# Performance work log

Measured on AMD Instinct MI355X. Metric: run time of the kernel, lower is better.

## Reference

```python
import jax, jax.numpy as jnp
import numpy as np

N_NODES = 50000
N_EDGES = 1600000
IN_DIM = 512
HID = 128  # conv1 out = 2*HID = 256, conv2 out = HID = 128
EPS = 1e-5


def gcn_conv(x, src, dst, W, b, n_nodes):
    """PyG GCNConv: x' = D^{-1/2} (A + I) D^{-1/2} (x W) + b (self loops added)."""
    h = x @ W  # [N, out]
    loop = jnp.arange(n_nodes, dtype=src.dtype)
    s = jnp.concatenate([src, loop])  # sources incl. self loops
    d = jnp.concatenate([dst, loop])  # targets incl. self loops
    ones = jnp.ones(s.shape[0], dtype=h.dtype)
    deg = jax.ops.segment_sum(ones, d, num_segments=n_nodes)  # in-degree on targets
    dis = jnp.where(deg > 0, jax.lax.rsqrt(jnp.maximum(deg, 1.0)), 0.0)
    norm = dis[s] * dis[d]  # [E+N]
    msg = norm[:, None] * h[s]  # gather + scale, [E+N, out]
    out = jax.ops.segment_sum(msg, d, num_segments=n_nodes)  # scatter-add
    return out + b


def batch_norm(x, gamma, beta):
    """BatchNorm1d with batch statistics (biased variance), eps=1e-5."""
    mean = jnp.mean(x, axis=0)
    var = jnp.mean(jnp.square(x - mean), axis=0)
    return (x - mean) * jax.lax.rsqrt(var + EPS) * gamma + beta


def setup_inputs() -> dict:
    key = jax.random.key(0)
    ks = jax.random.split(key, 8)
    x = jax.random.normal(ks[0], (N_NODES, IN_DIM), dtype=jnp.float32)
    edge_index = jax.random.randint(ks[1], (2, N_EDGES), 0, N_NODES, dtype=jnp.int64)
    d1 = 2 * HID
    W1 = jax.random.normal(ks[2], (IN_DIM, d1), dtype=jnp.float32) / np.sqrt(IN_DIM)
    b1 = jnp.zeros((d1,), dtype=jnp.float32)
    gamma1 = jnp.ones((d1,), dtype=jnp.float32)
    beta1 = jnp.zeros((d1,), dtype=jnp.float32)
    W2 = jax.random.normal(ks[3], (d1, HID), dtype=jnp.float32) / np.sqrt(d1)
    b2 = jnp.zeros((HID,), dtype=jnp.float32)
    gamma2 = jnp.ones((HID,), dtype=jnp.float32)
    beta2 = jnp.zeros((HID,), dtype=jnp.float32)
    return {"x": x, "edge_index": edge_index, "W1": W1, "b1": b1,
            "gamma1": gamma1, "beta1": beta1, "W2": W2, "b2": b2,
            "gamma2": gamma2, "beta2": beta2}


def reference(x, edge_index, W1, b1, gamma1, beta1, W2, b2, gamma2, beta2):
    src, dst = edge_index[0], edge_index[1]
    h = gcn_conv(x, src, dst, W1, b1, N_NODES)
    h = batch_norm(h, gamma1, beta1)
    h = jax.nn.relu(h)
    # dropout: identity in eval mode (deterministic reference)
    h = gcn_conv(h, src, dst, W2, b2, N_NODES)
    h = batch_norm(h, gamma2, beta2)
    return h
```

## Files before the change

kernel.cpp:

```cpp
#include <hip/hip_runtime.h>
#include <hip/hip_bf16.h>


#define NN 50000
#define NE 1600000
#define DIN 512
#define D1 256
#define D2 128
#define EPSV 1e-5f
#define NBUCK 8
#define BSZ 6250
#define NDB 128
#define NPB 391
#define CAP 16384

typedef __attribute__((ext_vector_type(8))) short bf16x8_t;
typedef __attribute__((ext_vector_type(4))) float f32x4_t;

__device__ __forceinline__ float bf2f(unsigned short u) {
  return __uint_as_float(((unsigned int)u) << 16);
}
__device__ __forceinline__ unsigned short f2bf(float f) {
  unsigned int u = __float_as_uint(f);
  u += 0x7fffu + ((u >> 16) & 1u);
  return (unsigned short)(u >> 16);
}
__device__ __forceinline__ unsigned int pk2(float a, float b) {
  __hip_bfloat162 h = __float22bfloat162_rn(make_float2(a, b));
  union { __hip_bfloat162 h; unsigned int u; } c;
  c.h = h;
  return c.u;
}

__global__ void k_zero(int* __restrict__ gcursor, float* __restrict__ stats) {
  int i = blockIdx.x * 256 + threadIdx.x;
  if (i < NDB) gcursor[i] = 0;
  if (i < (D1 * 2 + D2 * 2)) stats[i] = 0.0f;
}

__global__ __launch_bounds__(256) void k_part(const int* __restrict__ src,
                                              const int* __restrict__ dst,
                                              int* __restrict__ gcursor,
                                              unsigned int* __restrict__ part) {
  __shared__ int hist[NDB];
  __shared__ int curs[NDB];
  const int t = threadIdx.x;
  const int EB = NE / 256;
  const int e0 = blockIdx.x * EB;
  if (t < NDB) hist[t] = 0;
  __syncthreads();
  for (int i = t; i < EB; i += 256) {
    int d = dst[e0 + i];
    atomicAdd(&hist[d / NPB], 1);
  }
  __syncthreads();
  if (t < NDB) {
    int c = hist[t];
    curs[t] = (c > 0) ? atomicAdd(&gcursor[t], c) : 0;
  }
  __syncthreads();
  for (int i = t; i < EB; i += 256) {
    int s = src[e0 + i];
    int d = dst[e0 + i];
    int b = d / NPB;
    int dl = d - b * NPB;
    int sb = (unsigned)s / BSZ;
    unsigned int w = (unsigned)s | ((unsigned)dl << 16) | ((unsigned)sb << 25);
    int pos = atomicAdd(&curs[b], 1);
    if (pos < CAP) part[(size_t)b * CAP + pos] = w;
  }
}

__global__ void k_bscan(const int* __restrict__ gcursor, int* __restrict__ ebase) {
  __shared__ int s[NDB];
  int t = threadIdx.x;
  int v = gcursor[t];
  s[t] = v;
  __syncthreads();
  for (int off = 1; off < NDB; off <<= 1) {
    int a = (t >= off) ? s[t - off] : 0;
    __syncthreads();
    s[t] += a;
    __syncthreads();
  }
  ebase[t] = s[t] - v;
  if (t == NDB - 1) ebase[NDB] = s[t];
}

__global__ __launch_bounds__(256) void k_build(const unsigned int* __restrict__ part,
                                               const int* __restrict__ gcursor,
                                               const int* __restrict__ ebase,
                                               int* __restrict__ row_ptr,
                                               float* __restrict__ dis,
                                               int* __restrict__ col) {
  const int NC = NPB * NBUCK;
  __shared__ int cnt[NC];
  __shared__ int tsum[256];
  const int b = blockIdx.x, t = threadIdx.x;
  int m = gcursor[b];
  if (m > CAP) m = CAP;
  const int base = ebase[b];
  const unsigned int* my = part + (size_t)b * CAP;
  for (int i = t; i < NC; i += 256) cnt[i] = 0;
  __syncthreads();
  for (int i = t; i < m; i += 256) {
    unsigned int w = my[i];
    atomicAdd(&cnt[((w >> 16) & 0x1ff) * NBUCK + (w >> 25)], 1);
  }
  __syncthreads();
  const int CHK = (NC + 255) / 256;
  int i0 = t * CHK;
  int sum = 0;
  for (int i = 0; i < CHK; i++) {
    int idx = i0 + i;
    if (idx < NC) sum += cnt[idx];
  }
  tsum[t] = sum;
  __syncthreads();
  for (int off = 1; off < 256; off <<= 1) {
    int a = (t >= off) ? tsum[t - off] : 0;
    __syncthreads();
    tsum[t] += a;
    __syncthreads();
  }
  int run = tsum[t] - sum;
  for (int i = 0; i < CHK; i++) {
    int idx = i0 + i;
    if (idx < NC) {
      int c = cnt[idx];
      cnt[idx] = run;
      run += c;
    }
  }
  __syncthreads();
  const int n0 = b * NPB;
  for (int dl = t; dl < NPB; dl += 256) {
    int n = n0 + dl;
    if (n < NN) {
      int st = cnt[dl * NBUCK];
      int en = (dl * NBUCK + NBUCK < NC) ? cnt[dl * NBUCK + NBUCK] : m;
      row_ptr[n] = base + st;
      dis[n] = rsqrtf((float)(en - st + 1));
    }
  }
  if (b == NDB - 1 && t == 0) row_ptr[NN] = base + m;
  __syncthreads();
  for (int i = t; i < m; i += 256) {
    unsigned int w = my[i];
    int pos = atomicAdd(&cnt[((w >> 16) & 0x1ff) * NBUCK + (w >> 25)], 1);
    col[base + pos] = w & 0xffff;
  }
}

__global__ void k_prep_w(const float* __restrict__ W1, const float* __restrict__ W2,
                         unsigned short* __restrict__ W1t, unsigned short* __restrict__ W2t) {
  int i = blockIdx.x * 256 + threadIdx.x;
  if (i < DIN * D1) {
    int n = i / DIN, k = i - n * DIN;
    W1t[i] = f2bf(W1[(size_t)k * D1 + n]);
  } else {
    int j = i - DIN * D1;
    int n = j / D1, k = j - n * D1;
    W2t[j] = f2bf(W2[(size_t)k * D2 + n]);
  }
}

__global__ __launch_bounds__(512) void k_gemm1(const float* __restrict__ A,
                                               const unsigned short* __restrict__ Bt,
                                               unsigned short* __restrict__ C, int M) {
  __shared__ unsigned short As[128 * 64];
  __shared__ unsigned short Bs[256 * 64];
  const int t = threadIdx.x;
  const int wave = t >> 6, lane = t & 63;
  const int m0 = blockIdx.x * 128;
  const int wm = (wave & 1) * 64, wn = (wave >> 1) * 64;
  const int l8 = lane >> 3;
  const int lbs = (lane & 7) ^ l8;
  const int row_c = lane & 15, quad = lane >> 4;

  f32x4_t acc[4][4];
#pragma unroll
  for (int i = 0; i < 4; i++)
#pragma unroll
    for (int j = 0; j < 4; j++) acc[i][j] = (f32x4_t){0.f, 0.f, 0.f, 0.f};

  for (int k0 = 0; k0 < DIN; k0 += 64) {
#pragma unroll
    for (int j = 0; j < 4; j++) {
      int chunk = wave * 4 + j;
      int row = chunk * 8 + l8;
      const unsigned short* g = Bt + (size_t)row * DIN + k0 + lbs * 8;
      __builtin_amdgcn_global_load_lds(
          (const __attribute__((address_space(1))) unsigned int*)g,
          (__attribute__((address_space(3))) unsigned int*)(Bs + chunk * 512), 16, 0, 0);
    }
#pragma unroll
    for (int i = 0; i < 2; i++) {
      int bid = i * 512 + t;
      int row = bid >> 3, pb = bid & 7;
      int lb = pb ^ (row & 7);
      int gm = m0 + row;
      if (gm >= M) gm = M - 1;
      const float4* s = (const float4*)(A + (size_t)gm * DIN + k0 + lb * 8);
      float4 v0 = s[0], v1 = s[1];
      uint4 o;
      o.x = pk2(v0.x, v0.y);
      o.y = pk2(v0.z, v0.w);
      o.z = pk2(v1.x, v1.y);
      o.w = pk2(v1.z, v1.w);
      *(uint4*)(As + row * 64 + pb * 8) = o;
    }
    __syncthreads();
#pragma unroll
    for (int ki = 0; ki < 2; ki++) {
      bf16x8_t af[4], bfr[4];
      int kb = ki * 4 + quad;
#pragma unroll
      for (int i = 0; i < 4; i++) {
        int ar = wm + i * 16 + row_c;
        af[i] = *(const bf16x8_t*)(As + ar * 64 + ((kb ^ (ar & 7)) * 8));
        int br = wn + i * 16 + row_c;
        bfr[i] = *(const bf16x8_t*)(Bs + br * 64 + ((kb ^ (br & 7)) * 8));
      }
#pragma unroll
      for (int i = 0; i < 4; i++)
#pragma unroll
        for (int j = 0; j < 4; j++)
          acc[i][j] = __builtin_amdgcn_mfma_f32_16x16x32_bf16(af[i], bfr[j], acc[i][j], 0, 0, 0);
    }
    __syncthreads();
  }
#pragma unroll
  for (int i = 0; i < 4; i++) {
#pragma unroll
    for (int j = 0; j < 4; j++) {
      int colv = wn + j * 16 + row_c;
#pragma unroll
      for (int r = 0; r < 4; r++) {
        int gm = m0 + wm + i * 16 + quad * 4 + r;
        if (gm < M) C[(size_t)gm * D1 + colv] = f2bf(acc[i][j][r]);
      }
    }
  }
}

__global__ void k_finalize1(const float* __restrict__ stats, const float* __restrict__ gamma,
                            const float* __restrict__ beta, float* __restrict__ sc1,
                            float* __restrict__ sh1) {
  int c = threadIdx.x;
  float mean = stats[c] * (1.0f / NN);
  float var = stats[D1 + c] * (1.0f / NN) - mean * mean;
  float sc = gamma[c] * rsqrtf(var + EPSV);
  sc1[c] = sc;
  sh1[c] = beta[c] - mean * sc;
}

__global__ __launch_bounds__(256) void k_gemm2(const unsigned short* __restrict__ A,
                                               const float* __restrict__ sc1,
                                               const float* __restrict__ sh1,
                                               const unsigned short* __restrict__ Bt,
                                               unsigned short* __restrict__ C, int M) {
  __shared__ unsigned short As[128 * 64];
  __shared__ unsigned short Bs[128 * 64];
  const int t = threadIdx.x;
  const int wave = t >> 6, lane = t & 63;
  const int m0 = blockIdx.x * 128;
  const int wm = (wave >> 1) * 64, wn = (wave & 1) * 64;
  const int l8 = lane >> 3;
  const int lbs = (lane & 7) ^ l8;
  const int row_c = lane & 15, quad = lane >> 4;

  f32x4_t acc[4][4];
#pragma unroll
  for (int i = 0; i < 4; i++)
#pragma unroll
    for (int j = 0; j < 4; j++) acc[i][j] = (f32x4_t){0.f, 0.f, 0.f, 0.f};

  for (int k0 = 0; k0 < D1; k0 += 64) {
#pragma unroll
    for (int j = 0; j < 4; j++) {
      int chunk = wave * 4 + j;
      int row = chunk * 8 + l8;
      const unsigned short* g = Bt + (size_t)row * D1 + k0 + lbs * 8;
      __builtin_amdgcn_global_load_lds(
          (const __attribute__((address_space(1))) unsigned int*)g,
          (__attribute__((address_space(3))) unsigned int*)(Bs + chunk * 512), 16, 0, 0);
    }
#pragma unroll
    for (int i = 0; i < 4; i++) {
      int bid = i * 256 + t;
      int row = bid >> 3, pb = bid & 7;
      int lb = pb ^ (row & 7);
      int gm = m0 + row;
      if (gm >= M) gm = M - 1;
      int colb = k0 + lb * 8;
      uint4 raw = *(const uint4*)(A + (size_t)gm * D1 + colb);
      float4 scA = *(const float4*)(sc1 + colb);
      float4 scB = *(const float4*)(sc1 + colb + 4);
      float4 shA = *(const float4*)(sh1 + colb);
      float4 shB = *(const float4*)(sh1 + colb + 4);
      float f0 = fmaxf(fmaf(bf2f((unsigned short)(raw.x & 0xffff)), scA.x, shA.x), 0.f);
      float f1 = fmaxf(fmaf(bf2f((unsigned short)(raw.x >> 16)),    scA.y, shA.y), 0.f);
      float f2 = fmaxf(fmaf(bf2f((unsigned short)(raw.y & 0xffff)), scA.z, shA.z), 0.f);
      float f3 = fmaxf(fmaf(bf2f((unsigned short)(raw.y >> 16)),    scA.w, shA.w), 0.f);
      float f4 = fmaxf(fmaf(bf2f((unsigned short)(raw.z & 0xffff)), scB.x, shB.x), 0.f);
      float f5 = fmaxf(fmaf(bf2f((unsigned short)(raw.z >> 16)),    scB.y, shB.y), 0.f);
      float f6 = fmaxf(fmaf(bf2f((unsigned short)(raw.w & 0xffff)), scB.z, shB.z), 0.f);
      float f7 = fmaxf(fmaf(bf2f((unsigned short)(raw.w >> 16)),    scB.w, shB.w), 0.f);
      uint4 o;
      o.x = pk2(f0, f1);
      o.y = pk2(f2, f3);
      o.z = pk2(f4, f5);
      o.w = pk2(f6, f7);
      *(uint4*)(As + row * 64 + pb * 8) = o;
    }
    __syncthreads();
#pragma unroll
    for (int ki = 0; ki < 2; ki++) {
      bf16x8_t af[4], bfr[4];
      int kb = ki * 4 + quad;
#pragma unroll
      for (int i = 0; i < 4; i++) {
        int ar = wm + i * 16 + row_c;
        af[i] = *(const bf16x8_t*)(As + ar * 64 + ((kb ^ (ar & 7)) * 8));
        int br = wn + i * 16 + row_c;
        bfr[i] = *(const bf16x8_t*)(Bs + br * 64 + ((kb ^ (br & 7)) * 8));
      }
#pragma unroll
      for (int i = 0; i < 4; i++)
#pragma unroll
        for (int j = 0; j < 4; j++)
          acc[i][j] = __builtin_amdgcn_mfma_f32_16x16x32_bf16(af[i], bfr[j], acc[i][j], 0, 0, 0);
    }
    __syncthreads();
  }
#pragma unroll
  for (int i = 0; i < 4; i++) {
#pragma unroll
    for (int j = 0; j < 4; j++) {
      int colv = wn + j * 16 + row_c;
      if (colv < D2) {
#pragma unroll
        for (int r = 0; r < 4; r++) {
          int gm = m0 + wm + i * 16 + quad * 4 + r;
          if (gm < M) C[(size_t)gm * D2 + colv] = f2bf(acc[i][j][r]);
        }
      }
    }
  }
}

__global__ __launch_bounds__(256) void k_agg1(const unsigned short* __restrict__ H,
                                              const int* __restrict__ row_ptr,
                                              const int* __restrict__ col,
                                              const float* __restrict__ dis,
                                              const float* __restrict__ bias,
                                              unsigned short* __restrict__ OUT) {
  int n = blockIdx.x * 4 + (threadIdx.x >> 6);
  int lane = threadIdx.x & 63;
  if (n >= NN) return;
  float dn = dis[n];
  ushort4 v = ((const ushort4*)(H + (size_t)n * D1))[lane];
  float wsf = dn * dn;
  float a0 = wsf * bf2f(v.x), a1 = wsf * bf2f(v.y);
  float a2 = wsf * bf2f(v.z), a3 = wsf * bf2f(v.w);
  int e = row_ptr[n], e1 = row_ptr[n + 1];
  for (; e + 3 < e1; e += 4) {
    int s0 = col[e], s1 = col[e + 1], s2 = col[e + 2], s3 = col[e + 3];
    float w0 = dis[s0] * dn, w1 = dis[s1] * dn;
    float w2 = dis[s2] * dn, w3 = dis[s3] * dn;
    ushort4 u0 = ((const ushort4*)(H + (size_t)s0 * D1))[lane];
    ushort4 u1 = ((const ushort4*)(H + (size_t)s1 * D1))[lane];
    ushort4 u2 = ((const ushort4*)(H + (size_t)s2 * D1))[lane];
    ushort4 u3 = ((const ushort4*)(H + (size_t)s3 * D1))[lane];
    a0 += w0 * bf2f(u0.x) + w1 * bf2f(u1.x) + w2 * bf2f(u2.x) + w3 * bf2f(u3.x);
    a1 += w0 * bf2f(u0.y) + w1 * bf2f(u1.y) + w2 * bf2f(u2.y) + w3 * bf2f(u3.y);
    a2 += w0 * bf2f(u0.z) + w1 * bf2f(u1.z) + w2 * bf2f(u2.z) + w3 * bf2f(u3.z);
    a3 += w0 * bf2f(u0.w) + w1 * bf2f(u1.w) + w2 * bf2f(u2.w) + w3 * bf2f(u3.w);
  }
  for (; e < e1; e++) {
    int sa = col[e];
    float wa = dis[sa] * dn;
    ushort4 ua = ((const ushort4*)(H + (size_t)sa * D1))[lane];
    a0 += wa * bf2f(ua.x);
    a1 += wa * bf2f(ua.y);
    a2 += wa * bf2f(ua.z);
    a3 += wa * bf2f(ua.w);
  }
  int c = lane * 4;
  a0 += bias[c]; a1 += bias[c + 1]; a2 += bias[c + 2]; a3 += bias[c + 3];
  ushort4 o;
  o.x = f2bf(a0); o.y = f2bf(a1); o.z = f2bf(a2); o.w = f2bf(a3);
  ((ushort4*)(OUT + (size_t)n * D1))[lane] = o;
}

__global__ __launch_bounds__(256) void k_agg2(const unsigned short* __restrict__ H,
                                              const int* __restrict__ row_ptr,
                                              const int* __restrict__ col,
                                              const float* __restrict__ dis,
                                              const float* __restrict__ bias,
                                              float* __restrict__ OUT) {
  int n = blockIdx.x * 4 + (threadIdx.x >> 6);
  int lane = threadIdx.x & 63;
  if (n >= NN) return;
  float dn = dis[n];
  ushort2 v = ((const ushort2*)(H + (size_t)n * D2))[lane];
  float wsf = dn * dn;
  float a0 = wsf * bf2f(v.x), a1 = wsf * bf2f(v.y);
  int e = row_ptr[n], e1 = row_ptr[n + 1];
  for (; e + 3 < e1; e += 4) {
    int s0 = col[e], s1 = col[e + 1], s2 = col[e + 2], s3 = col[e + 3];
    float w0 = dis[s0] * dn, w1 = dis[s1] * dn;
    float w2 = dis[s2] * dn, w3 = dis[s3] * dn;
    ushort2 u0 = ((const ushort2*)(H + (size_t)s0 * D2))[lane];
    ushort2 u1 = ((const ushort2*)(H + (size_t)s1 * D2))[lane];
    ushort2 u2 = ((const ushort2*)(H + (size_t)s2 * D2))[lane];
    ushort2 u3 = ((const ushort2*)(H + (size_t)s3 * D2))[lane];
    a0 += w0 * bf2f(u0.x) + w1 * bf2f(u1.x) + w2 * bf2f(u2.x) + w3 * bf2f(u3.x);
    a1 += w0 * bf2f(u0.y) + w1 * bf2f(u1.y) + w2 * bf2f(u2.y) + w3 * bf2f(u3.y);
  }
  for (; e < e1; e++) {
    int sa = col[e];
    float wa = dis[sa] * dn;
    ushort2 ua = ((const ushort2*)(H + (size_t)sa * D2))[lane];
    a0 += wa * bf2f(ua.x);
    a1 += wa * bf2f(ua.y);
  }
  int c = lane * 2;
  a0 += bias[c]; a1 += bias[c + 1];
  ((float2*)(OUT + (size_t)n * D2))[lane] = make_float2(a0, a1);
}

__global__ void k_stats1(const unsigned short* __restrict__ X, float* __restrict__ stats) {
  int t = threadIdx.x;
  int r0 = blockIdx.x * 64;
  int r1 = (r0 + 64 < NN) ? r0 + 64 : NN;
  float s = 0.f, q = 0.f;
  for (int r = r0; r < r1; r++) {
    float v = bf2f(X[(size_t)r * D1 + t]);
    s += v;
    q += v * v;
  }
  atomicAdd(&stats[t], s);
  atomicAdd(&stats[D1 + t], q);
}

__global__ void k_stats2(const float* __restrict__ X, float* __restrict__ stats) {
  int t = threadIdx.x;
  int r0 = blockIdx.x * 128;
  int r1 = (r0 + 128 < NN) ? r0 + 128 : NN;
  float s = 0.f, q = 0.f;
  for (int r = r0; r < r1; r++) {
    float v = X[(size_t)r * D2 + t];
    s += v;
    q += v * v;
  }
  atomicAdd(&stats[t], s);
  atomicAdd(&stats[D2 + t], q);
}

__global__ void k_apply2(float* __restrict__ X, const float* __restrict__ stats,
                         const float* __restrict__ gamma, const float* __restrict__ beta) {
  int i = blockIdx.x * blockDim.x + threadIdx.x;
  int c = i & (D2 - 1);
  float mean = stats[c] * (1.0f / NN);
  float var = stats[D2 + c] * (1.0f / NN) - mean * mean;
  float sc = gamma[c] * rsqrtf(var + EPSV);
  X[i] = (X[i] - mean) * sc + beta[c];
}

extern "C" void kernel_launch(void* const* d_in, const int* in_sizes, int n_in,
                              void* d_out, int out_size, void* d_ws, size_t ws_size,
                              hipStream_t stream) {
  const float* x  = (const float*)d_in[0];
  const int* ei   = (const int*)d_in[1];
  const int* srcv = ei;
  const int* dstv = ei + NE;
  const float* W1  = (const float*)d_in[2];
  const float* b1  = (const float*)d_in[3];
  const float* g1  = (const float*)d_in[4];
  const float* be1 = (const float*)d_in[5];
  const float* W2  = (const float*)d_in[6];
  const float* b2  = (const float*)d_in[7];
  const float* g2  = (const float*)d_in[8];
  const float* be2 = (const float*)d_in[9];
  float* out = (float*)d_out;

  char* ws = (char*)d_ws;
  size_t off = 0;
  auto alloc = [&](size_t bytes) {
    size_t cur = off;
    off = (off + bytes + 255) & ~(size_t)255;
    return cur;
  };
  int* row_ptr   = (int*)(ws + alloc((NN + 1) * 4));
  float* dis     = (float*)(ws + alloc(NN * 4));
  int* gcursor   = (int*)(ws + alloc(NDB * 4));
  int* ebase     = (int*)(ws + alloc((NDB + 1) * 4));
  float* stats   = (float*)(ws + alloc((D1 * 2 + D2 * 2) * 4));
  float* sc1     = (float*)(ws + alloc(D1 * 4));
  float* sh1     = (float*)(ws + alloc(D1 * 4));
  int* col       = (int*)(ws + alloc((size_t)NE * 4));
  unsigned short* H1  = (unsigned short*)(ws + alloc((size_t)NN * D1 * 2));
  unsigned short* A1  = (unsigned short*)(ws + alloc((size_t)NN * D1 * 2));
  unsigned short* H2  = (unsigned short*)(ws + alloc((size_t)NN * D2 * 2));
  unsigned short* W1t = (unsigned short*)(ws + alloc((size_t)DIN * D1 * 2));
  unsigned short* W2t = (unsigned short*)(ws + alloc((size_t)D1 * D2 * 2));
  float* stats2 = stats + D1 * 2;
  unsigned int* part = (unsigned int*)H1;

  k_zero<<<3, 256, 0, stream>>>(gcursor, stats);
  k_part<<<256, 256, 0, stream>>>(srcv, dstv, gcursor, part);
  k_bscan<<<1, NDB, 0, stream>>>(gcursor, ebase);
  k_build<<<NDB, 256, 0, stream>>>(part, gcursor, ebase, row_ptr, dis, col);

  k_prep_w<<<(DIN * D1 + D1 * D2) / 256, 256, 0, stream>>>(W1, W2, W1t, W2t);

  const int mb = (NN + 127) / 128;

  k_gemm1<<<mb, 512, 0, stream>>>(x, W1t, H1, NN);
  k_agg1<<<(NN + 3) / 4, 256, 0, stream>>>(H1, row_ptr, col, dis, b1, A1);
  k_stats1<<<(NN + 63) / 64, 256, 0, stream>>>(A1, stats);
  k_finalize1<<<1, 256, 0, stream>>>(stats, g1, be1, sc1, sh1);

  k_gemm2<<<mb, 256, 0, stream>>>(A1, sc1, sh1, W2t, H2, NN);
  k_agg2<<<(NN + 3) / 4, 256, 0, stream>>>(H2, row_ptr, col, dis, b2, out);
  k_stats2<<<(NN + 127) / 128, 128, 0, stream>>>(out, stats2);
  k_apply2<<<NN * D2 / 256, 256, 0, stream>>>(out, stats2, g2, be2);
}
```

Measured before the change: 529.8 us.

## Cooperatively load edge indices per wave and broadcast via readlane in aggregation

In both aggregation kernels, each wave now loads up to 64 neighbor indices and their normalization weights in one coalesced load, one per lane. It then broadcasts them with readlane and issues 8 row gathers at a time. This replaces the redundant per-lane loads of col and dis and raises memory-level parallelism for the gathers. It also doubles the bucket count and halves the bucket size used by the CSR build, which changes the sort/partition granularity. The cost is more registers per thread and some extra readlane instructions.

```diff
diff --git a/kernel.cpp b/kernel.cpp
--- a/kernel.cpp
+++ b/kernel.cpp
@@ -8,8 +8,8 @@
 #define D1 256
 #define D2 128
 #define EPSV 1e-5f
-#define NBUCK 8
-#define BSZ 6250
+#define NBUCK 16
+#define BSZ 3125
 #define NDB 128
 #define NPB 391
 #define CAP 16384
@@ -365,27 +365,44 @@
   float a0 = wsf * bf2f(v.x), a1 = wsf * bf2f(v.y);
   float a2 = wsf * bf2f(v.z), a3 = wsf * bf2f(v.w);
   int e = row_ptr[n], e1 = row_ptr[n + 1];
-  for (; e + 3 < e1; e += 4) {
-    int s0 = col[e], s1 = col[e + 1], s2 = col[e + 2], s3 = col[e + 3];
-    float w0 = dis[s0] * dn, w1 = dis[s1] * dn;
-    float w2 = dis[s2] * dn, w3 = dis[s3] * dn;
-    ushort4 u0 = ((const ushort4*)(H + (size_t)s0 * D1))[lane];
-    ushort4 u1 = ((const ushort4*)(H + (size_t)s1 * D1))[lane];
-    ushort4 u2 = ((const ushort4*)(H + (size_t)s2 * D1))[lane];
-    ushort4 u3 = ((const ushort4*)(H + (size_t)s3 * D1))[lane];
-    a0 += w0 * bf2f(u0.x) + w1 * bf2f(u1.x) + w2 * bf2f(u2.x) + w3 * bf2f(u3.x);
-    a1 += w0 * bf2f(u0.y) + w1 * bf2f(u1.y) + w2 * bf2f(u2.y) + w3 * bf2f(u3.y);
-    a2 += w0 * bf2f(u0.z) + w1 * bf2f(u1.z) + w2 * bf2f(u2.z) + w3 * bf2f(u3.z);
-    a3 += w0 * bf2f(u0.w) + w1 * bf2f(u1.w) + w2 * bf2f(u2.w) + w3 * bf2f(u3.w);
-  }
-  for (; e < e1; e++) {
-    int sa = col[e];
-    float wa = dis[sa] * dn;
-    ushort4 ua = ((const ushort4*)(H + (size_t)sa * D1))[lane];
-    a0 += wa * bf2f(ua.x);
-    a1 += wa * bf2f(ua.y);
-    a2 += wa * bf2f(ua.z);
-    a3 += wa * bf2f(ua.w);
+  while (e < e1) {
+    int cnt = e1 - e;
+    if (cnt > 64) cnt = 64;
+    int li = (lane < cnt) ? lane : (cnt - 1);
+    int cv = col[e + li];
+    float dwv = dis[cv] * dn;
+    int dwu = __float_as_int(dwv);
+    int b = 0;
+    for (; b + 8 <= cnt; b += 8) {
+      int s[8];
+      float w[8];
+      ushort4 u[8];
+#pragma unroll
+      for (int k = 0; k < 8; k++) {
+        s[k] = __builtin_amdgcn_readlane(cv, b + k);
+        w[k] = __int_as_float(__builtin_amdgcn_readlane(dwu, b + k));
+      }
+#pragma unroll
+      for (int k = 0; k < 8; k++)
+        u[k] = ((const ushort4*)(H + (size_t)s[k] * D1))[lane];
+#pragma unroll
+      for (int k = 0; k < 8; k++) {
+        a0 += w[k] * bf2f(u[k].x);
+        a1 += w[k] * bf2f(u[k].y);
+        a2 += w[k] * bf2f(u[k].z);
+        a3 += w[k] * bf2f(u[k].w);
+      }
+    }
+    for (; b < cnt; b++) {
+      int sK = __builtin_amdgcn_readlane(cv, b);
+      float wK = __int_as_float(__builtin_amdgcn_readlane(dwu, b));
+      ushort4 uK = ((const ushort4*)(H + (size_t)sK * D1))[lane];
+      a0 += wK * bf2f(uK.x);
+      a1 += wK * bf2f(uK.y);
+      a2 += wK * bf2f(uK.z);
+      a3 += wK * bf2f(uK.w);
+    }
+    e += cnt;
   }
   int c = lane * 4;
   a0 += bias[c]; a1 += bias[c + 1]; a2 += bias[c + 2]; a3 += bias[c + 3];
@@ -408,23 +425,40 @@
   float wsf = dn * dn;
   float a0 = wsf * bf2f(v.x), a1 = wsf * bf2f(v.y);
   int e = row_ptr[n], e1 = row_ptr[n + 1];
-  for (; e + 3 < e1; e += 4) {
-    int s0 = col[e], s1 = col[e + 1], s2 = col[e + 2], s3 = col[e + 3];
-    float w0 = dis[s0] * dn, w1 = dis[s1] * dn;
-    float w2 = dis[s2] * dn, w3 = dis[s3] * dn;
-    ushort2 u0 = ((const ushort2*)(H + (size_t)s0 * D2))[lane];
-    ushort2 u1 = ((const ushort2*)(H + (size_t)s1 * D2))[lane];
-    ushort2 u2 = ((const ushort2*)(H + (size_t)s2 * D2))[lane];
-    ushort2 u3 = ((const ushort2*)(H + (size_t)s3 * D2))[lane];
-    a0 += w0 * bf2f(u0.x) + w1 * bf2f(u1.x) + w2 * bf2f(u2.x) + w3 * bf2f(u3.x);
-    a1 += w0 * bf2f(u0.y) + w1 * bf2f(u1.y) + w2 * bf2f(u2.y) + w3 * bf2f(u3.y);
-  }
-  for (; e < e1; e++) {
-    int sa = col[e];
-    float wa = dis[sa] * dn;
-    ushort2 ua = ((const ushort2*)(H + (size_t)sa * D2))[lane];
-    a0 += wa * bf2f(ua.x);
-    a1 += wa * bf2f(ua.y);
+  while (e < e1) {
+    int cnt = e1 - e;
+    if (cnt > 64) cnt = 64;
+    int li = (lane < cnt) ? lane : (cnt - 1);
+    int cv = col[e + li];
+    float dwv = dis[cv] * dn;
+    int dwu = __float_as_int(dwv);
+    int b = 0;
+    for (; b + 8 <= cnt; b += 8) {
+      int s[8];
+      float w[8];
+      ushort2 u[8];
+#pragma unroll
+      for (int k = 0; k < 8; k++) {
+        s[k] = __builtin_amdgcn_readlane(cv, b + k);
+        w[k] = __int_as_float(__builtin_amdgcn_readlane(dwu, b + k));
+      }
+#pragma unroll
+      for (int k = 0; k < 8; k++)
+        u[k] = ((const ushort2*)(H + (size_t)s[k] * D2))[lane];
+#pragma unroll
+      for (int k = 0; k < 8; k++) {
+        a0 += w[k] * bf2f(u[k].x);
+        a1 += w[k] * bf2f(u[k].y);
+      }
+    }
+    for (; b < cnt; b++) {
+      int sK = __builtin_amdgcn_readlane(cv, b);
+      float wK = __int_as_float(__builtin_amdgcn_readlane(dwu, b));
+      ushort2 uK = ((const ushort2*)(H + (size_t)sK * D2))[lane];
+      a0 += wK * bf2f(uK.x);
+      a1 += wK * bf2f(uK.y);
+    }
+    e += cnt;
   }
   int c = lane * 2;
   a0 += bias[c]; a1 += bias[c + 1];
```

Result: faster. 512.9 us (-3.2%).

## Aggregate many nodes per wave bucket-by-bucket for source locality

Applied to the files above, without the earlier changes.

The CSR build now records per-node boundaries for 16 source buckets instead of a single row pointer. Each aggregation wave owns 13 destination nodes and walks all of them one source bucket at a time, with block-wide barriers between buckets. The aim is to keep concurrently gathered source rows in a narrow range so they hit L2/MALL, and to fold the destination normalisation into the epilogue. The cost is a larger boundary array, heavy register use for 13 accumulators per wave, a much smaller grid that gives less parallelism, and barrier stalls that can leave waves waiting.

```diff
diff --git a/kernel.cpp b/kernel.cpp
--- a/kernel.cpp
+++ b/kernel.cpp
@@ -8,11 +8,14 @@
 #define D1 256
 #define D2 128
 #define EPSV 1e-5f
-#define NBUCK 8
-#define BSZ 6250
+#define NBUCK 16
+#define BSZ 3125
 #define NDB 128
 #define NPB 391
 #define CAP 16384
+
+#define AGG_KN 13
+#define AGG_GRID ((NN + AGG_KN * 4 - 1) / (AGG_KN * 4))
 
 typedef __attribute__((ext_vector_type(8))) short bf16x8_t;
 typedef __attribute__((ext_vector_type(4))) float f32x4_t;
@@ -90,7 +93,7 @@
 __global__ __launch_bounds__(256) void k_build(const unsigned int* __restrict__ part,
                                                const int* __restrict__ gcursor,
                                                const int* __restrict__ ebase,
-                                               int* __restrict__ row_ptr,
+                                               int* __restrict__ bptr,
                                                float* __restrict__ dis,
                                                int* __restrict__ col) {
   const int NC = NPB * NBUCK;
@@ -134,16 +137,20 @@
   }
   __syncthreads();
   const int n0 = b * NPB;
+  for (int i = t; i < NC; i += 256) {
+    int dl = i >> 4;
+    int n = n0 + dl;
+    if (n < NN) bptr[(size_t)n * NBUCK + (i & 15)] = base + cnt[i];
+  }
   for (int dl = t; dl < NPB; dl += 256) {
     int n = n0 + dl;
     if (n < NN) {
       int st = cnt[dl * NBUCK];
       int en = (dl * NBUCK + NBUCK < NC) ? cnt[dl * NBUCK + NBUCK] : m;
-      row_ptr[n] = base + st;
       dis[n] = rsqrtf((float)(en - st + 1));
     }
   }
-  if (b == NDB - 1 && t == 0) row_ptr[NN] = base + m;
+  if (b == NDB - 1 && t == 0) bptr[(size_t)NN * NBUCK] = base + m;
   __syncthreads();
   for (int i = t; i < m; i += 256) {
     unsigned int w = my[i];
@@ -350,85 +357,165 @@
   }
 }
 
-__global__ __launch_bounds__(256) void k_agg1(const unsigned short* __restrict__ H,
-                                              const int* __restrict__ row_ptr,
-                                              const int* __restrict__ col,
-                                              const float* __restrict__ dis,
-                                              const float* __restrict__ bias,
-                                              unsigned short* __restrict__ OUT) {
-  int n = blockIdx.x * 4 + (threadIdx.x >> 6);
-  int lane = threadIdx.x & 63;
-  if (n >= NN) return;
-  float dn = dis[n];
-  ushort4 v = ((const ushort4*)(H + (size_t)n * D1))[lane];
-  float wsf = dn * dn;
-  float a0 = wsf * bf2f(v.x), a1 = wsf * bf2f(v.y);
-  float a2 = wsf * bf2f(v.z), a3 = wsf * bf2f(v.w);
-  int e = row_ptr[n], e1 = row_ptr[n + 1];
-  for (; e + 3 < e1; e += 4) {
-    int s0 = col[e], s1 = col[e + 1], s2 = col[e + 2], s3 = col[e + 3];
-    float w0 = dis[s0] * dn, w1 = dis[s1] * dn;
-    float w2 = dis[s2] * dn, w3 = dis[s3] * dn;
-    ushort4 u0 = ((const ushort4*)(H + (size_t)s0 * D1))[lane];
-    ushort4 u1 = ((const ushort4*)(H + (size_t)s1 * D1))[lane];
-    ushort4 u2 = ((const ushort4*)(H + (size_t)s2 * D1))[lane];
-    ushort4 u3 = ((const ushort4*)(H + (size_t)s3 * D1))[lane];
-    a0 += w0 * bf2f(u0.x) + w1 * bf2f(u1.x) + w2 * bf2f(u2.x) + w3 * bf2f(u3.x);
-    a1 += w0 * bf2f(u0.y) + w1 * bf2f(u1.y) + w2 * bf2f(u2.y) + w3 * bf2f(u3.y);
-    a2 += w0 * bf2f(u0.z) + w1 * bf2f(u1.z) + w2 * bf2f(u2.z) + w3 * bf2f(u3.z);
-    a3 += w0 * bf2f(u0.w) + w1 * bf2f(u1.w) + w2 * bf2f(u2.w) + w3 * bf2f(u3.w);
-  }
-  for (; e < e1; e++) {
-    int sa = col[e];
-    float wa = dis[sa] * dn;
-    ushort4 ua = ((const ushort4*)(H + (size_t)sa * D1))[lane];
-    a0 += wa * bf2f(ua.x);
-    a1 += wa * bf2f(ua.y);
-    a2 += wa * bf2f(ua.z);
-    a3 += wa * bf2f(ua.w);
-  }
-  int c = lane * 4;
-  a0 += bias[c]; a1 += bias[c + 1]; a2 += bias[c + 2]; a3 += bias[c + 3];
-  ushort4 o;
-  o.x = f2bf(a0); o.y = f2bf(a1); o.z = f2bf(a2); o.w = f2bf(a3);
-  ((ushort4*)(OUT + (size_t)n * D1))[lane] = o;
-}
-
-__global__ __launch_bounds__(256) void k_agg2(const unsigned short* __restrict__ H,
-                                              const int* __restrict__ row_ptr,
-                                              const int* __restrict__ col,
-                                              const float* __restrict__ dis,
-                                              const float* __restrict__ bias,
-                                              float* __restrict__ OUT) {
-  int n = blockIdx.x * 4 + (threadIdx.x >> 6);
-  int lane = threadIdx.x & 63;
-  if (n >= NN) return;
-  float dn = dis[n];
-  ushort2 v = ((const ushort2*)(H + (size_t)n * D2))[lane];
-  float wsf = dn * dn;
-  float a0 = wsf * bf2f(v.x), a1 = wsf * bf2f(v.y);
-  int e = row_ptr[n], e1 = row_ptr[n + 1];
-  for (; e + 3 < e1; e += 4) {
-    int s0 = col[e], s1 = col[e + 1], s2 = col[e + 2], s3 = col[e + 3];
-    float w0 = dis[s0] * dn, w1 = dis[s1] * dn;
-    float w2 = dis[s2] * dn, w3 = dis[s3] * dn;
-    ushort2 u0 = ((const ushort2*)(H + (size_t)s0 * D2))[lane];
-    ushort2 u1 = ((const ushort2*)(H + (size_t)s1 * D2))[lane];
-    ushort2 u2 = ((const ushort2*)(H + (size_t)s2 * D2))[lane];
-    ushort2 u3 = ((const ushort2*)(H + (size_t)s3 * D2))[lane];
-    a0 += w0 * bf2f(u0.x) + w1 * bf2f(u1.x) + w2 * bf2f(u2.x) + w3 * bf2f(u3.x);
-    a1 += w0 * bf2f(u0.y) + w1 * bf2f(u1.y) + w2 * bf2f(u2.y) + w3 * bf2f(u3.y);
-  }
-  for (; e < e1; e++) {
-    int sa = col[e];
-    float wa = dis[sa] * dn;
-    ushort2 ua = ((const ushort2*)(H + (size_t)sa * D2))[lane];
-    a0 += wa * bf2f(ua.x);
-    a1 += wa * bf2f(ua.y);
-  }
-  int c = lane * 2;
-  a0 += bias[c]; a1 += bias[c + 1];
-  ((float2*)(OUT + (size_t)n * D2))[lane] = make_float2(a0, a1);
+__global__ __launch_bounds__(256, 4) void k_agg1(const unsigned short* __restrict__ H,
+                                                 const int* __restrict__ bptr,
+                                                 const int* __restrict__ col,
+                                                 const float* __restrict__ dis,
+                                                 const float* __restrict__ bias,
+                                                 unsigned short* __restrict__ OUT) {
+  const int lane = threadIdx.x & 63;
+  const int wid = blockIdx.x * 4 + (threadIdx.x >> 6);
+  const int n0 = wid * AGG_KN;
+
+  float a0[AGG_KN], a1[AGG_KN], a2[AGG_KN], a3[AGG_KN];
+  int bnd[AGG_KN];
+
+#pragma unroll
+  for (int j = 0; j < AGG_KN; j++) {
+    int n = n0 + j;
+    if (n < NN) {
+      float d = dis[n];
+      ushort4 v = ((const ushort4*)(H + (size_t)n * D1))[lane];
+      a0[j] = d * bf2f(v.x); a1[j] = d * bf2f(v.y);
+      a2[j] = d * bf2f(v.z); a3[j] = d * bf2f(v.w);
+      int li = (lane <= NBUCK) ? lane : NBUCK;
+      bnd[j] = bptr[(size_t)n * NBUCK + li];
+    } else {
+      a0[j] = a1[j] = a2[j] = a3[j] = 0.f;
+      bnd[j] = 0;
+    }
+  }
+
+  for (int b = 0; b < NBUCK; b++) {
+#pragma unroll
+    for (int j = 0; j < AGG_KN; j++) {
+      int s = __builtin_amdgcn_readlane(bnd[j], b);
+      int e = __builtin_amdgcn_readlane(bnd[j], b + 1);
+      for (; s + 4 <= e; s += 4) {
+        int c0 = col[s], c1 = col[s + 1], c2 = col[s + 2], c3 = col[s + 3];
+        float w0 = dis[c0], w1 = dis[c1], w2 = dis[c2], w3 = dis[c3];
+        ushort4 u0 = ((const ushort4*)(H + (size_t)c0 * D1))[lane];
+        ushort4 u1 = ((const ushort4*)(H + (size_t)c1 * D1))[lane];
+        ushort4 u2 = ((const ushort4*)(H + (size_t)c2 * D1))[lane];
+        ushort4 u3 = ((const ushort4*)(H + (size_t)c3 * D1))[lane];
+        a0[j] += w0 * bf2f(u0.x) + w1 * bf2f(u1.x) + w2 * bf2f(u2.x) + w3 * bf2f(u3.x);
+        a1[j] += w0 * bf2f(u0.y) + w1 * bf2f(u1.y) + w2 * bf2f(u2.y) + w3 * bf2f(u3.y);
+        a2[j] += w0 * bf2f(u0.z) + w1 * bf2f(u1.z) + w2 * bf2f(u2.z) + w3 * bf2f(u3.z);
+        a3[j] += w0 * bf2f(u0.w) + w1 * bf2f(u1.w) + w2 * bf2f(u2.w) + w3 * bf2f(u3.w);
+      }
+      if (s + 2 <= e) {
+        int c0 = col[s], c1 = col[s + 1];
+        float w0 = dis[c0], w1 = dis[c1];
+        ushort4 u0 = ((const ushort4*)(H + (size_t)c0 * D1))[lane];
+        ushort4 u1 = ((const ushort4*)(H + (size_t)c1 * D1))[lane];
+        a0[j] += w0 * bf2f(u0.x) + w1 * bf2f(u1.x);
+        a1[j] += w0 * bf2f(u0.y) + w1 * bf2f(u1.y);
+        a2[j] += w0 * bf2f(u0.z) + w1 * bf2f(u1.z);
+        a3[j] += w0 * bf2f(u0.w) + w1 * bf2f(u1.w);
+        s += 2;
+      }
+      if (s < e) {
+        int c0 = col[s];
+        float w0 = dis[c0];
+        ushort4 u0 = ((const ushort4*)(H + (size_t)c0 * D1))[lane];
+        a0[j] += w0 * bf2f(u0.x);
+        a1[j] += w0 * bf2f(u0.y);
+        a2[j] += w0 * bf2f(u0.z);
+        a3[j] += w0 * bf2f(u0.w);
+      }
+    }
+    __syncthreads();
+  }
+
+  float4 bb = ((const float4*)bias)[lane];
+#pragma unroll
+  for (int j = 0; j < AGG_KN; j++) {
+    int n = n0 + j;
+    if (n < NN) {
+      float d = dis[n];
+      ushort4 o;
+      o.x = f2bf(fmaf(d, a0[j], bb.x));
+      o.y = f2bf(fmaf(d, a1[j], bb.y));
+      o.z = f2bf(fmaf(d, a2[j], bb.z));
+      o.w = f2bf(fmaf(d, a3[j], bb.w));
+      ((ushort4*)(OUT + (size_t)n * D1))[lane] = o;
+    }
+  }
+}
+
+__global__ __launch_bounds__(256, 4) void k_agg2(const unsigned short* __restrict__ H,
+                                                 const int* __restrict__ bptr,
+                                                 const int* __restrict__ col,
+                                                 const float* __restrict__ dis,
+                                                 const float* __restrict__ bias,
+                                                 float* __restrict__ OUT) {
+  const int lane = threadIdx.x & 63;
+  const int wid = blockIdx.x * 4 + (threadIdx.x >> 6);
+  const int n0 = wid * AGG_KN;
+
+  float a0[AGG_KN], a1[AGG_KN];
+  int bnd[AGG_KN];
+
+#pragma unroll
+  for (int j = 0; j < AGG_KN; j++) {
+    int n = n0 + j;
+    if (n < NN) {
+      float d = dis[n];
+      ushort2 v = ((const ushort2*)(H + (size_t)n * D2))[lane];
+      a0[j] = d * bf2f(v.x); a1[j] = d * bf2f(v.y);
+      int li = (lane <= NBUCK) ? lane : NBUCK;
+      bnd[j] = bptr[(size_t)n * NBUCK + li];
+    } else {
+      a0[j] = a1[j] = 0.f;
+      bnd[j] = 0;
+    }
+  }
+
+  for (int b = 0; b < NBUCK; b++) {
+#pragma unroll
+    for (int j = 0; j < AGG_KN; j++) {
+      int s = __builtin_amdgcn_readlane(bnd[j], b);
+      int e = __builtin_amdgcn_readlane(bnd[j], b + 1);
+      for (; s + 4 <= e; s += 4) {
+        int c0 = col[s], c1 = col[s + 1], c2 = col[s + 2], c3 = col[s + 3];
+        float w0 = dis[c0], w1 = dis[c1], w2 = dis[c2], w3 = dis[c3];
+        ushort2 u0 = ((const ushort2*)(H + (size_t)c0 * D2))[lane];
+        ushort2 u1 = ((const ushort2*)(H + (size_t)c1 * D2))[lane];
+        ushort2 u2 = ((const ushort2*)(H + (size_t)c2 * D2))[lane];
+        ushort2 u3 = ((const ushort2*)(H + (size_t)c3 * D2))[lane];
+        a0[j] += w0 * bf2f(u0.x) + w1 * bf2f(u1.x) + w2 * bf2f(u2.x) + w3 * bf2f(u3.x);
+        a1[j] += w0 * bf2f(u0.y) + w1 * bf2f(u1.y) + w2 * bf2f(u2.y) + w3 * bf2f(u3.y);
+      }
+      if (s + 2 <= e) {
+        int c0 = col[s], c1 = col[s + 1];
+        float w0 = dis[c0], w1 = dis[c1];
+        ushort2 u0 = ((const ushort2*)(H + (size_t)c0 * D2))[lane];
+        ushort2 u1 = ((const ushort2*)(H + (size_t)c1 * D2))[lane];
+        a0[j] += w0 * bf2f(u0.x) + w1 * bf2f(u1.x);
+        a1[j] += w0 * bf2f(u0.y) + w1 * bf2f(u1.y);
+        s += 2;
+      }
+      if (s < e) {
+        int c0 = col[s];
+        float w0 = dis[c0];
+        ushort2 u0 = ((const ushort2*)(H + (size_t)c0 * D2))[lane];
+        a0[j] += w0 * bf2f(u0.x);
+        a1[j] += w0 * bf2f(u0.y);
+      }
+    }
+    __syncthreads();
+  }
+
+  float2 bb = ((const float2*)bias)[lane];
+#pragma unroll
+  for (int j = 0; j < AGG_KN; j++) {
+    int n = n0 + j;
+    if (n < NN) {
+      float d = dis[n];
+      ((float2*)(OUT + (size_t)n * D2))[lane] =
+          make_float2(fmaf(d, a0[j], bb.x), fmaf(d, a1[j], bb.y));
+    }
+  }
 }
 
 __global__ void k_stats1(const unsigned short* __restrict__ X, float* __restrict__ stats) {
@@ -493,13 +580,13 @@
     off = (off + bytes + 255) & ~(size_t)255;
     return cur;
   };
-  int* row_ptr   = (int*)(ws + alloc((NN + 1) * 4));
   float* dis     = (float*)(ws + alloc(NN * 4));
   int* gcursor   = (int*)(ws + alloc(NDB * 4));
   int* ebase     = (int*)(ws + alloc((NDB + 1) * 4));
   float* stats   = (float*)(ws + alloc((D1 * 2 + D2 * 2) * 4));
   float* sc1     = (float*)(ws + alloc(D1 * 4));
   float* sh1     = (float*)(ws + alloc(D1 * 4));
+  int* bptr      = (int*)(ws + alloc(((size_t)NN * NBUCK + 1) * 4));
   int* col       = (int*)(ws + alloc((size_t)NE * 4));
   unsigned short* H1  = (unsigned short*)(ws + alloc((size_t)NN * D1 * 2));
   unsigned short* A1  = (unsigned short*)(ws + alloc((size_t)NN * D1 * 2));
@@ -512,19 +599,19 @@
   k_zero<<<3, 256, 0, stream>>>(gcursor, stats);
   k_part<<<256, 256, 0, stream>>>(srcv, dstv, gcursor, part);
   k_bscan<<<1, NDB, 0, stream>>>(gcursor, ebase);
-  k_build<<<NDB, 256, 0, stream>>>(part, gcursor, ebase, row_ptr, dis, col);
+  k_build<<<NDB, 256, 0, stream>>>(part, gcursor, ebase, bptr, dis, col);
 
   k_prep_w<<<(DIN * D1 + D1 * D2) / 256, 256, 0, stream>>>(W1, W2, W1t, W2t);
 
   const int mb = (NN + 127) / 128;
 
   k_gemm1<<<mb, 512, 0, stream>>>(x, W1t, H1, NN);
-  k_agg1<<<(NN + 3) / 4, 256, 0, stream>>>(H1, row_ptr, col, dis, b1, A1);
+  k_agg1<<<AGG_GRID, 256, 0, stream>>>(H1, bptr, col, dis, b1, A1);
   k_stats1<<<(NN + 63) / 64, 256, 0, stream>>>(A1, stats);
   k_finalize1<<<1, 256, 0, stream>>>(stats, g1, be1, sc1, sh1);
 
   k_gemm2<<<mb, 256, 0, stream>>>(A1, sc1, sh1, W2t, H2, NN);
-  k_agg2<<<(NN + 3) / 4, 256, 0, stream>>>(H2, row_ptr, col, dis, b2, out);
+  k_agg2<<<AGG_GRID, 256, 0, stream>>>(H2, bptr, col, dis, b2, out);
   k_stats2<<<(NN + 127) / 128, 128, 0, stream>>>(out, stats2);
   k_apply2<<<NN * D2 / 256, 256, 0, stream>>>(out, stats2, g2, be2);
 }
```

Result: slower. 653.5 us (+23.3%).
